# Kernel tuning notes

Hardware: AMD Instinct MI355X
Metric: run time of the kernel (lower is better)

## Reference

```python
import jax, jax.numpy as jnp
import numpy as np

N_HEAD = 16
N_KV_HEAD = 4
HEAD_DIM = 128
EPS = 1e-6


def apply_rotary_emb(x, cos, sin):
    # x: (B,T,H,hd); cos/sin: (1,T,1,hd//2)
    d = x.shape[3] // 2
    x1, x2 = x[..., :d], x[..., d:]
    y1 = x1 * cos + x2 * sin
    y2 = x1 * -sin + x2 * cos
    return jnp.concatenate([y1, y2], axis=3).astype(x.dtype)


def rmsnorm(x):
    # flax nnx.RMSNorm with use_scale=False: x * rsqrt(mean(x^2) + eps)
    ms = jnp.mean(jnp.square(x), axis=-1, keepdims=True)
    return (x * jax.lax.rsqrt(ms + EPS)).astype(x.dtype)


def setup_inputs() -> dict:
    key = jax.random.key(0)
    ks = jax.random.split(key, 7)
    B, T, C = 4, 2048, 2048
    s = 0.02
    return {
        "x": jax.random.normal(ks[0], (B, T, C), jnp.float32),
        "cos": jax.random.normal(ks[1], (1, T, 1, HEAD_DIM // 2), jnp.float32),
        "sin": jax.random.normal(ks[2], (1, T, 1, HEAD_DIM // 2), jnp.float32),
        "Wq": jax.random.normal(ks[3], (C, N_HEAD * HEAD_DIM), jnp.float32) * s,
        "Wk": jax.random.normal(ks[4], (C, N_KV_HEAD * HEAD_DIM), jnp.float32) * s,
        "Wv": jax.random.normal(ks[5], (C, N_KV_HEAD * HEAD_DIM), jnp.float32) * s,
        "Wo": jax.random.normal(ks[6], (C, C), jnp.float32) * s,
    }


def reference(x, cos, sin, Wq, Wk, Wv, Wo):
    B, T, C = x.shape
    q = (x @ Wq).reshape(B, T, N_HEAD, HEAD_DIM)
    k = (x @ Wk).reshape(B, T, N_KV_HEAD, HEAD_DIM)
    v = (x @ Wv).reshape(B, T, N_KV_HEAD, HEAD_DIM)
    q = rmsnorm(apply_rotary_emb(q, cos, sin))
    k = rmsnorm(apply_rotary_emb(k, cos, sin))
    # (B,H,T,hd)
    q = jnp.transpose(q, (0, 2, 1, 3))
    k = jnp.transpose(k, (0, 2, 1, 3))
    v = jnp.transpose(v, (0, 2, 1, 3))
    nrep = N_HEAD // N_KV_HEAD
    k = jnp.repeat(k, nrep, axis=1)
    v = jnp.repeat(v, nrep, axis=1)
    scale = 1.0 / jnp.sqrt(jnp.float32(HEAD_DIM))
    att = jnp.einsum('bhqd,bhkd->bhqk', q, k) * scale
    mask = jnp.tril(jnp.ones((T, T), dtype=bool))[None, None, :, :]
    att = jnp.where(mask, att, -jnp.inf)
    att = jax.nn.softmax(att, axis=-1)
    y = jnp.einsum('bhqk,bhkd->bhqd', att, v)
    y = jnp.transpose(y, (0, 2, 1, 3)).reshape(B, T, -1)
    return y @ Wo
```

## Files before the change

### kernel.cpp

```cpp
#include <hip/hip_runtime.h>
#include <hip/hip_bf16.h>

typedef __attribute__((ext_vector_type(8))) short short8;
typedef __attribute__((ext_vector_type(4))) float f32x4;
typedef __attribute__((ext_vector_type(16))) float f32x16;

#define B_SZ 4
#define T_SEQ 2048
#define C_DIM 2048
#define NH 16
#define NKV 4
#define HD 128

#define MFMA16 __builtin_amdgcn_mfma_f32_16x16x32_bf16
#define MFMA32 __builtin_amdgcn_mfma_f32_32x32x16_bf16

__device__ __forceinline__ unsigned short f2bf(float f) {
  union { __hip_bfloat16 h; unsigned short u; } v;
  v.h = __float2bfloat16(f);
  return v.u;
}
__device__ __forceinline__ float bf2f(unsigned short u) {
  union { unsigned short u; __hip_bfloat16 h; } v;
  v.u = u;
  return __bfloat162float(v.h);
}
__device__ __forceinline__ unsigned pkbf(float lo, float hi) {
  return (unsigned)f2bf(lo) | ((unsigned)f2bf(hi) << 16);
}

__device__ __forceinline__ void gload_lds16(const unsigned short* g, unsigned short* l) {
  __builtin_amdgcn_global_load_lds(
      (const __attribute__((address_space(1))) unsigned int*)g,
      (__attribute__((address_space(3))) unsigned int*)l, 16, 0, 0);
}

__global__ void prep(const float* __restrict__ x, unsigned short* __restrict__ xb,
                     const float* __restrict__ Wq, const float* __restrict__ Wk,
                     const float* __restrict__ Wv, const float* __restrict__ Wo,
                     unsigned short* __restrict__ WqkvT, unsigned short* __restrict__ WoT) {
  int bid = blockIdx.x, tid = threadIdx.x;
  if (bid < 16384) {
    int i = bid * 256 + tid;
    float4 f = ((const float4*)x)[i];
    ushort4 u = make_ushort4(f2bf(f.x), f2bf(f.y), f2bf(f.z), f2bf(f.w));
    ((ushort4*)xb)[i] = u;
    return;
  }
  __shared__ float tile[32][33];
  int idx = bid - 16384;
  int y = idx >> 6, kx = idx & 63;
  const float* W;
  unsigned short* Wt;
  int N, n0;
  if (y < 64) { W = Wq; Wt = WqkvT; N = 2048; n0 = y * 32; }
  else if (y < 80) { W = Wk; Wt = WqkvT + (size_t)2048 * 2048; N = 512; n0 = (y - 64) * 32; }
  else if (y < 96) { W = Wv; Wt = WqkvT + (size_t)2560 * 2048; N = 512; n0 = (y - 80) * 32; }
  else { W = Wo; Wt = WoT; N = 2048; n0 = (y - 96) * 32; }
  int k0 = kx * 32;
  int tx = tid & 31, ty = tid >> 5;
#pragma unroll
  for (int i = 0; i < 4; i++)
    tile[ty + i * 8][tx] = W[(size_t)(k0 + ty + i * 8) * N + n0 + tx];
  __syncthreads();
#pragma unroll
  for (int i = 0; i < 4; i++)
    Wt[(size_t)(n0 + ty + i * 8) * 2048 + k0 + tx] = f2bf(tile[tx][ty + i * 8]);
}

__global__ void vtrans(const unsigned short* __restrict__ qkv, unsigned short* __restrict__ Vt) {
  __shared__ unsigned short tile[32][34];
  int t0 = blockIdx.x * 32, d0 = blockIdx.y * 32;
  int b = blockIdx.z >> 2, kvh = blockIdx.z & 3;
  int tx = threadIdx.x, ty = threadIdx.y;
#pragma unroll
  for (int i = 0; i < 4; i++)
    tile[ty + i * 8][tx] =
        qkv[(size_t)(b * T_SEQ + t0 + ty + i * 8) * 3072 + 2560 + kvh * HD + d0 + tx];
  __syncthreads();
#pragma unroll
  for (int i = 0; i < 4; i++)
    Vt[((size_t)(b * NKV + kvh) * HD + d0 + ty + i * 8) * T_SEQ + t0 + tx] = tile[tx][ty + i * 8];
}

template <typename OutT>
__global__ __launch_bounds__(512, 2) void gemm128(const unsigned short* __restrict__ A,
                                                  const unsigned short* __restrict__ Bt,
                                                  OutT* __restrict__ Cc, int N, int K, int GX) {
  __shared__ alignas(16) unsigned short lds[2][3][128 * 64];
  const int tid = threadIdx.x, lane = tid & 63, wid = tid >> 6;
  const int wave_m = wid >> 2, wave_n = wid & 3;
  const int r16 = lane & 15, q4 = lane >> 4;
  const int sw = r16 & 7;

  int nwg = gridDim.x, orig = blockIdx.x;
  int qq = nwg >> 3, rr = nwg & 7;
  int xcd = orig & 7, loc = orig >> 3;
  int wg = (xcd < rr ? xcd * (qq + 1) : rr * (qq + 1) + (xcd - rr) * qq) + loc;
  int bx = wg % GX, by = wg / GX;
  const size_t row0 = (size_t)bx * 128, col0 = (size_t)by * 256;

  const unsigned short* Ab = A + row0 * K;
  const unsigned short* Bb0 = Bt + col0 * K;
  const unsigned short* Bb1 = Bt + (col0 + 128) * K;

  const int srow = lane >> 3, spb = lane & 7;
  auto stage = [&](const unsigned short* base, int buf, int slot, int k0) {
#pragma unroll
    for (int j = 0; j < 2; ++j) {
      int cw = j * 8 + wid;
      int row = cw * 8 + srow;
      gload_lds16(base + (size_t)row * K + k0 + ((spb ^ srow) * 8), &lds[buf][slot][cw * 512]);
    }
  };

  f32x4 acc[4][4];
  f32x4 zero = {0.f, 0.f, 0.f, 0.f};
#pragma unroll
  for (int m = 0; m < 4; m++)
#pragma unroll
    for (int n = 0; n < 4; n++) acc[m][n] = zero;

  const int NT = K / 64;
  stage(Ab, 0, 0, 0);
  stage(Bb0, 0, 1, 0);
  stage(Bb1, 0, 2, 0);
  stage(Ab, 1, 0, 64);
  asm volatile("s_waitcnt vmcnt(2)" ::: "memory");
  __builtin_amdgcn_s_barrier();

  short8 af[4][2], b01[2][2], b23[2][2];
  const int bslot = 1 + (wave_n >> 1);
  const int bro = (wave_n & 1) * 64;

  int cur = 0;
#pragma unroll 1
  for (int t = 0; t < NT; ++t) {
    const unsigned short* Ah = &lds[cur][0][0];
    const unsigned short* Bh = &lds[cur][bslot][0];
    const int k1 = t * 64 + 64, k2 = t * 64 + 128;
#pragma unroll
    for (int mf = 0; mf < 4; mf++)
#pragma unroll
      for (int kk = 0; kk < 2; kk++)
        af[mf][kk] =
            *(const short8*)(Ah + (wave_m * 64 + mf * 16 + r16) * 64 + (((kk * 4 + q4) ^ sw) * 8));
#pragma unroll
    for (int nf = 0; nf < 2; nf++)
#pragma unroll
      for (int kk = 0; kk < 2; kk++)
        b01[nf][kk] =
            *(const short8*)(Bh + (bro + nf * 16 + r16) * 64 + (((kk * 4 + q4) ^ sw) * 8));
    if (t + 1 < NT) stage(Bb0, cur ^ 1, 1, k1);
    __builtin_amdgcn_s_barrier();
    asm volatile("s_waitcnt lgkmcnt(0)" ::: "memory");
    __builtin_amdgcn_s_setprio(1);
#pragma unroll
    for (int mf = 0; mf < 4; mf++)
#pragma unroll
      for (int nf = 0; nf < 2; nf++)
#pragma unroll
        for (int kk = 0; kk < 2; kk++)
          acc[mf][nf] = MFMA16(af[mf][kk], b01[nf][kk], acc[mf][nf], 0, 0, 0);
    __builtin_amdgcn_s_setprio(0);
    __builtin_amdgcn_s_barrier();
#pragma unroll
    for (int nf = 0; nf < 2; nf++)
#pragma unroll
      for (int kk = 0; kk < 2; kk++)
        b23[nf][kk] =
            *(const short8*)(Bh + (bro + (nf + 2) * 16 + r16) * 64 + (((kk * 4 + q4) ^ sw) * 8));
    if (t + 1 < NT) stage(Bb1, cur ^ 1, 2, k1);
    if (t + 2 < NT) stage(Ab, cur, 0, k2);
    __builtin_amdgcn_s_barrier();
    asm volatile("s_waitcnt lgkmcnt(0)" ::: "memory");
    __builtin_amdgcn_s_setprio(1);
#pragma unroll
    for (int mf = 0; mf < 4; mf++)
#pragma unroll
      for (int nf = 0; nf < 2; nf++)
#pragma unroll
        for (int kk = 0; kk < 2; kk++)
          acc[mf][nf + 2] = MFMA16(af[mf][kk], b23[nf][kk], acc[mf][nf + 2], 0, 0, 0);
    __builtin_amdgcn_s_setprio(0);
    if (t + 2 < NT)
      asm volatile("s_waitcnt vmcnt(2)" ::: "memory");
    else if (t + 1 < NT)
      asm volatile("s_waitcnt vmcnt(0)" ::: "memory");
    __builtin_amdgcn_s_barrier();
    cur ^= 1;
  }

#pragma unroll
  for (int mf = 0; mf < 4; mf++)
#pragma unroll
    for (int nf = 0; nf < 4; nf++) {
      size_t rbase = row0 + wave_m * 64 + mf * 16 + q4 * 4;
      size_t cc = col0 + wave_n * 64 + nf * 16 + r16;
#pragma unroll
      for (int jj = 0; jj < 4; jj++) {
        if constexpr (sizeof(OutT) == 2)
          Cc[(rbase + jj) * (size_t)N + cc] = f2bf(acc[mf][nf][jj]);
        else
          Cc[(rbase + jj) * (size_t)N + cc] = acc[mf][nf][jj];
      }
    }
}

template <typename OutT>
__global__ __launch_bounds__(512, 2) void gemm256(const unsigned short* __restrict__ A,
                                                  const unsigned short* __restrict__ Bt,
                                                  OutT* __restrict__ Cc, int N, int K, int GX) {
  __shared__ alignas(16) unsigned short lds[2][4][128 * 64];
  const int tid = threadIdx.x, lane = tid & 63, wid = tid >> 6;
  const int wave_m = wid >> 2, wave_n = wid & 3;
  const int r16 = lane & 15, q4 = lane >> 4;
  const int sw = r16 & 7;

  int nwg = gridDim.x, orig = blockIdx.x;
  int qq = nwg >> 3, rr = nwg & 7;
  int xcd = orig & 7, loc = orig >> 3;
  int wg = (xcd < rr ? xcd * (qq + 1) : rr * (qq + 1) + (xcd - rr) * qq) + loc;
  int bx = wg % GX, by = wg / GX;
  const size_t row0 = (size_t)bx * 256, col0 = (size_t)by * 256;

  const unsigned short* Ab0 = A + row0 * K;
  const unsigned short* Ab1 = A + (row0 + 128) * K;
  const unsigned short* Bb0 = Bt + col0 * K;
  const unsigned short* Bb1 = Bt + (col0 + 128) * K;

  const int srow = lane >> 3, spb = lane & 7;
  auto stage = [&](const unsigned short* base, int buf, int slot, int k0) {
#pragma unroll
    for (int j = 0; j < 2; ++j) {
      int cw = j * 8 + wid;
      int row = cw * 8 + srow;
      gload_lds16(base + (size_t)row * K + k0 + ((spb ^ srow) * 8), &lds[buf][slot][cw * 512]);
    }
  };

  f32x4 acc[8][4];
  f32x4 zero = {0.f, 0.f, 0.f, 0.f};
#pragma unroll
  for (int m = 0; m < 8; m++)
#pragma unroll
    for (int n = 0; n < 4; n++) acc[m][n] = zero;

  const int NT = K / 64;
  stage(Ab0, 0, 0, 0);
  stage(Ab1, 0, 1, 0);
  stage(Bb0, 0, 2, 0);
  stage(Bb1, 0, 3, 0);
  stage(Ab0, 1, 0, 64);
  stage(Ab1, 1, 1, 64);
  asm volatile("s_waitcnt vmcnt(4)" ::: "memory");
  __builtin_amdgcn_s_barrier();

  short8 af[4][2], b01[2][2], b23[2][2];
  const int bslot = 2 + (wave_n >> 1);
  const int bro = (wave_n & 1) * 64;

  int cur = 0;
#pragma unroll 1
  for (int t = 0; t < NT; ++t) {
    const unsigned short* Ah = &lds[cur][wave_m][0];
    const unsigned short* Bh = &lds[cur][bslot][0];
    const int k1 = t * 64 + 64, k2 = t * 64 + 128;
#pragma unroll
    for (int mf = 0; mf < 4; mf++)
#pragma unroll
      for (int kk = 0; kk < 2; kk++)
        af[mf][kk] = *(const short8*)(Ah + (mf * 16 + r16) * 64 + (((kk * 4 + q4) ^ sw) * 8));
#pragma unroll
    for (int nf = 0; nf < 2; nf++)
#pragma unroll
      for (int kk = 0; kk < 2; kk++)
        b01[nf][kk] =
            *(const short8*)(Bh + (bro + nf * 16 + r16) * 64 + (((kk * 4 + q4) ^ sw) * 8));
    if (t + 1 < NT) stage(Bb0, cur ^ 1, 2, k1);
    __builtin_amdgcn_s_barrier();
    asm volatile("s_waitcnt lgkmcnt(0)" ::: "memory");
    __builtin_amdgcn_s_setprio(1);
#pragma unroll
    for (int mf = 0; mf < 4; mf++)
#pragma unroll
      for (int nf = 0; nf < 2; nf++)
#pragma unroll
        for (int kk = 0; kk < 2; kk++)
          acc[mf][nf] = MFMA16(af[mf][kk], b01[nf][kk], acc[mf][nf], 0, 0, 0);
    __builtin_amdgcn_s_setprio(0);
    __builtin_amdgcn_s_barrier();
#pragma unroll
    for (int nf = 0; nf < 2; nf++)
#pragma unroll
      for (int kk = 0; kk < 2; kk++)
        b23[nf][kk] =
            *(const short8*)(Bh + (bro + (nf + 2) * 16 + r16) * 64 + (((kk * 4 + q4) ^ sw) * 8));
    if (t + 1 < NT) stage(Bb1, cur ^ 1, 3, k1);
    __builtin_amdgcn_s_barrier();
    asm volatile("s_waitcnt lgkmcnt(0)" ::: "memory");
    __builtin_amdgcn_s_setprio(1);
#pragma unroll
    for (int mf = 0; mf < 4; mf++)
#pragma unroll
      for (int nf = 0; nf < 2; nf++)
#pragma unroll
        for (int kk = 0; kk < 2; kk++)
          acc[mf][nf + 2] = MFMA16(af[mf][kk], b23[nf][kk], acc[mf][nf + 2], 0, 0, 0);
    __builtin_amdgcn_s_setprio(0);
    __builtin_amdgcn_s_barrier();
#pragma unroll
    for (int mf = 0; mf < 4; mf++)
#pragma unroll
      for (int kk = 0; kk < 2; kk++)
        af[mf][kk] =
            *(const short8*)(Ah + ((mf + 4) * 16 + r16) * 64 + (((kk * 4 + q4) ^ sw) * 8));
    __builtin_amdgcn_s_barrier();
    asm volatile("s_waitcnt lgkmcnt(0)" ::: "memory");
    __builtin_amdgcn_s_setprio(1);
#pragma unroll
    for (int mf = 0; mf < 4; mf++)
#pragma unroll
      for (int nf = 0; nf < 2; nf++)
#pragma unroll
        for (int kk = 0; kk < 2; kk++)
          acc[mf + 4][nf] = MFMA16(af[mf][kk], b01[nf][kk], acc[mf + 4][nf], 0, 0, 0);
    __builtin_amdgcn_s_setprio(0);
    __builtin_amdgcn_s_barrier();
    if (t + 2 < NT) {
      stage(Ab0, cur, 0, k2);
      stage(Ab1, cur, 1, k2);
    }
    __builtin_amdgcn_s_barrier();
    __builtin_amdgcn_s_setprio(1);
#pragma unroll
    for (int mf = 0; mf < 4; mf++)
#pragma unroll
      for (int nf = 0; nf < 2; nf++)
#pragma unroll
        for (int kk = 0; kk < 2; kk++)
          acc[mf + 4][nf + 2] = MFMA16(af[mf][kk], b23[nf][kk], acc[mf + 4][nf + 2], 0, 0, 0);
    __builtin_amdgcn_s_setprio(0);
    if (t + 1 < NT) {
      if (t + 2 < NT)
        asm volatile("s_waitcnt vmcnt(4)" ::: "memory");
      else
        asm volatile("s_waitcnt vmcnt(0)" ::: "memory");
    }
    __builtin_amdgcn_s_barrier();
    cur ^= 1;
  }

#pragma unroll
  for (int mf = 0; mf < 8; mf++)
#pragma unroll
    for (int nf = 0; nf < 4; nf++) {
      size_t rbase = row0 + wave_m * 128 + mf * 16 + q4 * 4;
      size_t cc = col0 + wave_n * 64 + nf * 16 + r16;
#pragma unroll
      for (int jj = 0; jj < 4; jj++) {
        if constexpr (sizeof(OutT) == 2)
          Cc[(rbase + jj) * (size_t)N + cc] = f2bf(acc[mf][nf][jj]);
        else
          Cc[(rbase + jj) * (size_t)N + cc] = acc[mf][nf][jj];
      }
    }
}

__global__ void ropeAll(const unsigned short* __restrict__ qkv, const float* __restrict__ cosp,
                        const float* __restrict__ sinp, unsigned short* __restrict__ Qb,
                        unsigned short* __restrict__ Kb) {
  int gid = blockIdx.x * 4 + (threadIdx.x >> 6);
  int lane = threadIdx.x & 63;
  int hh = gid % 20;
  int bt = gid / 20;
  int t = bt % T_SEQ, b = bt / T_SEQ;
  int colbase;
  unsigned short* dst;
  float outscale;
  if (hh < 16) {
    colbase = hh * HD;
    dst = Qb + ((size_t)(b * NH + hh) * T_SEQ + t) * HD;
    outscale = 0.08838834764831845f;
  } else {
    int h2 = hh - 16;
    colbase = 2048 + h2 * HD;
    dst = Kb + ((size_t)(b * NKV + h2) * T_SEQ + t) * HD;
    outscale = 1.0f;
  }
  const unsigned short* src = qkv + (size_t)(b * T_SEQ + t) * 3072 + colbase;
  float x1 = bf2f(src[lane]), x2 = bf2f(src[64 + lane]);
  float c = cosp[t * 64 + lane], s = sinp[t * 64 + lane];
  float y1 = x1 * c + x2 * s;
  float y2 = x2 * c - x1 * s;
  float ss = y1 * y1 + y2 * y2;
#pragma unroll
  for (int d = 1; d < 64; d <<= 1) ss += __shfl_xor(ss, d);
  float r = rsqrtf(ss * (1.f / 128.f) + 1e-6f) * outscale;
  dst[lane] = f2bf(y1 * r);
  dst[64 + lane] = f2bf(y2 * r);
}

__global__ __launch_bounds__(256, 2) void attn(const unsigned short* __restrict__ Qn,
                                               const unsigned short* __restrict__ Kn,
                                               const unsigned short* __restrict__ Vt,
                                               unsigned short* __restrict__ Y) {
  __shared__ alignas(16) unsigned short lK[2][32 * 128];
  __shared__ alignas(16) unsigned short lV[2][128 * 32];

  int lin = blockIdx.x;
  int low3 = lin & 7, rest = lin >> 3;
  int chi = rest >> 6, idx = rest & 63;
  int c = (chi << 3) | low3;
  int b = c >> 2, kvh = c & 3;
  int h = kvh * 4 + (idx >> 4);
  int qt = 15 - (idx & 15);
  int Q0 = qt * 128;

  int lane = threadIdx.x & 63, w = threadIdx.x >> 6;
  const int q5 = lane & 31, hi = lane >> 5;
  const int qrow = Q0 + w * 32 + q5;
  const unsigned short* Qp = Qn + ((size_t)(b * NH + h) * T_SEQ + qrow) * HD;
  const unsigned short* Kp = Kn + (size_t)(b * NKV + kvh) * T_SEQ * HD;
  const unsigned short* Vp = Vt + (size_t)(b * NKV + kvh) * HD * T_SEQ;

  short8 qf[8];
#pragma unroll
  for (int i = 0; i < 8; i++) qf[i] = *(const short8*)(Qp + i * 16 + hi * 8);

  f32x16 o4[4];
#pragma unroll
  for (int d = 0; d < 4; d++)
#pragma unroll
    for (int r = 0; r < 16; r++) o4[d][r] = 0.f;
  float mrow = -1e30f, Lp = 0.f;

  auto stageK = [&](int kv0, int buf) {
#pragma unroll
    for (int j = 0; j < 2; ++j) {
      int cw = w * 2 + j;
      int gi = cw * 64 + lane;
      int slot = gi >> 5, krow = gi & 31;
      gload_lds16(Kp + (size_t)(kv0 + krow) * HD + slot * 8, &lK[buf][cw * 512]);
    }
  };
  auto stageV = [&](int kv0, int buf) {
#pragma unroll
    for (int j = 0; j < 2; ++j) {
      int cw = w * 2 + j;
      int gi = cw * 64 + lane;
      int cb = gi >> 7, vrow = gi & 127;
      gload_lds16(Vp + (size_t)vrow * T_SEQ + kv0 + cb * 8, &lV[buf][cw * 512]);
    }
  };

  const int ntiles = 4 * qt + 4;
  const int ntw = (Q0 + w * 32 + 63) >> 5;

  stageK(0, 0);
  stageV(0, 0);
  __syncthreads();
  int cur = 0;

  for (int t = 0; t < ntiles; ++t) {
    int kv0 = t * 32;
    if (t + 1 < ntiles) { stageK(kv0 + 32, cur ^ 1); stageV(kv0 + 32, cur ^ 1); }
    if (t < ntw) {
      f32x16 st;
#pragma unroll
      for (int r = 0; r < 16; r++) st[r] = 0.f;
      __builtin_amdgcn_s_setprio(1);
#pragma unroll
      for (int i = 0; i < 8; i++) {
        short8 kf = *(const short8*)(&lK[cur][((2 * i + hi) * 32 + q5) * 8]);
        st = MFMA32(kf, qf[i], st, 0, 0, 0);
      }
      __builtin_amdgcn_s_setprio(0);
      if (kv0 + 31 > Q0 + w * 32) {
#pragma unroll
        for (int r = 0; r < 16; r++) {
          int kg = kv0 + (r & 3) + 8 * (r >> 2) + 4 * hi;
          if (kg > qrow) st[r] = -1e30f;
        }
      }
      float pm = st[0];
#pragma unroll
      for (int r = 1; r < 16; r++) pm = fmaxf(pm, st[r]);
      pm = fmaxf(pm, __shfl_xor(pm, 32));
      if (!__all(pm - mrow <= 8.0f)) {
        float mn = fmaxf(mrow, pm);
        float al = __expf(mrow - mn);
        mrow = mn;
        Lp *= al;
#pragma unroll
        for (int d = 0; d < 4; d++)
#pragma unroll
          for (int r = 0; r < 16; r++) o4[d][r] *= al;
      }
      float p[16];
#pragma unroll
      for (int r = 0; r < 16; r++) {
        p[r] = __expf(st[r] - mrow);
        Lp += p[r];
      }
#pragma unroll
      for (int ks = 0; ks < 2; ks++) {
        unsigned x0 = pkbf(p[8 * ks + 0], p[8 * ks + 1]);
        unsigned x1 = pkbf(p[8 * ks + 2], p[8 * ks + 3]);
        unsigned y0 = pkbf(p[8 * ks + 4], p[8 * ks + 5]);
        unsigned y1 = pkbf(p[8 * ks + 6], p[8 * ks + 7]);
        unsigned sx0 = __shfl_xor((int)x0, 32), sx1 = __shfl_xor((int)x1, 32);
        unsigned sy0 = __shfl_xor((int)y0, 32), sy1 = __shfl_xor((int)y1, 32);
        union { unsigned u[4]; short8 s; } pw;
        pw.u[0] = hi ? sy0 : x0;
        pw.u[1] = hi ? sy1 : x1;
        pw.u[2] = hi ? y0 : sx0;
        pw.u[3] = hi ? y1 : sx1;
        const int cb = 2 * ks + hi;
        __builtin_amdgcn_s_setprio(1);
#pragma unroll
        for (int db = 0; db < 4; db++) {
          short8 vf = *(const short8*)(&lV[cur][(cb * 128 + db * 32 + q5) * 8]);
          o4[db] = MFMA32(vf, pw.s, o4[db], 0, 0, 0);
        }
        __builtin_amdgcn_s_setprio(0);
      }
    }
    __syncthreads();
    cur ^= 1;
  }

  float L = Lp + __shfl_xor(Lp, 32);
  float linv = 1.f / L;
  unsigned short* Yp = Y + ((size_t)(b * T_SEQ) + qrow) * (NH * HD) + h * HD;
#pragma unroll
  for (int db = 0; db < 4; db++)
#pragma unroll
    for (int g = 0; g < 4; g++) {
      int d0 = db * 32 + g * 8 + 4 * hi;
      ushort4 v = make_ushort4(f2bf(o4[db][g * 4 + 0] * linv), f2bf(o4[db][g * 4 + 1] * linv),
                               f2bf(o4[db][g * 4 + 2] * linv), f2bf(o4[db][g * 4 + 3] * linv));
      *(ushort4*)(Yp + d0) = v;
    }
}

extern "C" void kernel_launch(void* const* d_in, const int* in_sizes, int n_in,
                              void* d_out, int out_size, void* d_ws, size_t ws_size,
                              hipStream_t stream) {
  const float* x = (const float*)d_in[0];
  const float* cosp = (const float*)d_in[1];
  const float* sinp = (const float*)d_in[2];
  const float* Wq = (const float*)d_in[3];
  const float* Wk = (const float*)d_in[4];
  const float* Wv = (const float*)d_in[5];
  const float* Wo = (const float*)d_in[6];
  float* out = (float*)d_out;

  char* ws = (char*)d_ws;
  size_t off = 0;
  auto alloc = [&](size_t bytes) { void* p = ws + off; off += bytes; return p; };
  const size_t BT = (size_t)B_SZ * T_SEQ;
  unsigned short* xb = (unsigned short*)alloc(BT * C_DIM * 2);
  unsigned short* WqkvT = (unsigned short*)alloc((size_t)3072 * 2048 * 2);
  unsigned short* WoT = (unsigned short*)alloc((size_t)2048 * 2048 * 2);
  unsigned short* qkv = (unsigned short*)alloc(BT * 3072 * 2);
  unsigned short* Kb = (unsigned short*)alloc(BT * 512 * 2);
  unsigned short* Vb = (unsigned short*)alloc(BT * 512 * 2);
  unsigned short* Qb = xb;
  unsigned short* Yb = qkv;

  dim3 tb(32, 8);
  prep<<<26624, 256, 0, stream>>>(x, xb, Wq, Wk, Wv, Wo, WqkvT, WoT);

  gemm128<unsigned short><<<768, 512, 0, stream>>>(xb, WqkvT, qkv, 3072, 2048, 64);

  ropeAll<<<(B_SZ * T_SEQ * 20) / 4, 256, 0, stream>>>(qkv, cosp, sinp, Qb, Kb);
  vtrans<<<dim3(64, 4, 16), tb, 0, stream>>>(qkv, Vb);

  attn<<<dim3(1024), 256, 0, stream>>>(Qb, Kb, Vb, Yb);

  gemm256<float><<<256, 512, 0, stream>>>(Yb, WoT, out, 2048, 2048, 32);
}
```

Before: 404.5 us.

## Load attention K/V straight to registers and merge rope with V transpose

The attention kernel drops its LDS double-buffered K/V staging and block-wide barriers. Each wave now loads its own K and V fragments directly from global memory into registers and prefetches the next K tile during softmax. Each wave also loops only over its own causal tile count, not the block-wide count. Separately, the rope/norm kernel and the V transpose kernel are merged into one launch to save a launch. The trade-off is that the four waves sharing a KV head no longer share loads, so global/L2 traffic and register pressure rise.

```diff
diff --git a/kernel.cpp b/kernel.cpp
--- a/kernel.cpp
+++ b/kernel.cpp
@@ -68,21 +68,6 @@
     Wt[(size_t)(n0 + ty + i * 8) * 2048 + k0 + tx] = f2bf(tile[tx][ty + i * 8]);
 }
 
-__global__ void vtrans(const unsigned short* __restrict__ qkv, unsigned short* __restrict__ Vt) {
-  __shared__ unsigned short tile[32][34];
-  int t0 = blockIdx.x * 32, d0 = blockIdx.y * 32;
-  int b = blockIdx.z >> 2, kvh = blockIdx.z & 3;
-  int tx = threadIdx.x, ty = threadIdx.y;
-#pragma unroll
-  for (int i = 0; i < 4; i++)
-    tile[ty + i * 8][tx] =
-        qkv[(size_t)(b * T_SEQ + t0 + ty + i * 8) * 3072 + 2560 + kvh * HD + d0 + tx];
-  __syncthreads();
-#pragma unroll
-  for (int i = 0; i < 4; i++)
-    Vt[((size_t)(b * NKV + kvh) * HD + d0 + ty + i * 8) * T_SEQ + t0 + tx] = tile[tx][ty + i * 8];
-}
-
 template <typename OutT>
 __global__ __launch_bounds__(512, 2) void gemm128(const unsigned short* __restrict__ A,
                                                   const unsigned short* __restrict__ Bt,
@@ -367,47 +352,63 @@
     }
 }
 
-__global__ void ropeAll(const unsigned short* __restrict__ qkv, const float* __restrict__ cosp,
-                        const float* __restrict__ sinp, unsigned short* __restrict__ Qb,
-                        unsigned short* __restrict__ Kb) {
-  int gid = blockIdx.x * 4 + (threadIdx.x >> 6);
-  int lane = threadIdx.x & 63;
-  int hh = gid % 20;
-  int bt = gid / 20;
-  int t = bt % T_SEQ, b = bt / T_SEQ;
-  int colbase;
-  unsigned short* dst;
-  float outscale;
-  if (hh < 16) {
-    colbase = hh * HD;
-    dst = Qb + ((size_t)(b * NH + hh) * T_SEQ + t) * HD;
-    outscale = 0.08838834764831845f;
-  } else {
-    int h2 = hh - 16;
-    colbase = 2048 + h2 * HD;
-    dst = Kb + ((size_t)(b * NKV + h2) * T_SEQ + t) * HD;
-    outscale = 1.0f;
+__global__ void ropevt(const unsigned short* __restrict__ qkv, const float* __restrict__ cosp,
+                       const float* __restrict__ sinp, unsigned short* __restrict__ Qb,
+                       unsigned short* __restrict__ Kb, unsigned short* __restrict__ Vt) {
+  int bid = blockIdx.x, tid = threadIdx.x;
+  if (bid < 40960) {
+    int gid = bid * 4 + (tid >> 6);
+    int lane = tid & 63;
+    int hh = gid % 20;
+    int bt = gid / 20;
+    int t = bt % T_SEQ, b = bt / T_SEQ;
+    int colbase;
+    unsigned short* dst;
+    float outscale;
+    if (hh < 16) {
+      colbase = hh * HD;
+      dst = Qb + ((size_t)(b * NH + hh) * T_SEQ + t) * HD;
+      outscale = 0.08838834764831845f;
+    } else {
+      int h2 = hh - 16;
+      colbase = 2048 + h2 * HD;
+      dst = Kb + ((size_t)(b * NKV + h2) * T_SEQ + t) * HD;
+      outscale = 1.0f;
+    }
+    const unsigned short* src = qkv + (size_t)(b * T_SEQ + t) * 3072 + colbase;
+    float x1 = bf2f(src[lane]), x2 = bf2f(src[64 + lane]);
+    float c = cosp[t * 64 + lane], s = sinp[t * 64 + lane];
+    float y1 = x1 * c + x2 * s;
+    float y2 = x2 * c - x1 * s;
+    float ss = y1 * y1 + y2 * y2;
+#pragma unroll
+    for (int d = 1; d < 64; d <<= 1) ss += __shfl_xor(ss, d);
+    float r = rsqrtf(ss * (1.f / 128.f) + 1e-6f) * outscale;
+    dst[lane] = f2bf(y1 * r);
+    dst[64 + lane] = f2bf(y2 * r);
+    return;
   }
-  const unsigned short* src = qkv + (size_t)(b * T_SEQ + t) * 3072 + colbase;
-  float x1 = bf2f(src[lane]), x2 = bf2f(src[64 + lane]);
-  float c = cosp[t * 64 + lane], s = sinp[t * 64 + lane];
-  float y1 = x1 * c + x2 * s;
-  float y2 = x2 * c - x1 * s;
-  float ss = y1 * y1 + y2 * y2;
-#pragma unroll
-  for (int d = 1; d < 64; d <<= 1) ss += __shfl_xor(ss, d);
-  float r = rsqrtf(ss * (1.f / 128.f) + 1e-6f) * outscale;
-  dst[lane] = f2bf(y1 * r);
-  dst[64 + lane] = f2bf(y2 * r);
+  __shared__ unsigned short tile[32][34];
+  int idx = bid - 40960;
+  int xg = idx & 63, rem = idx >> 6;
+  int yg = rem & 3, zg = rem >> 2;
+  int t0 = xg * 32, d0 = yg * 32;
+  int b = zg >> 2, kvh = zg & 3;
+  int tx = tid & 31, ty = tid >> 5;
+#pragma unroll
+  for (int i = 0; i < 4; i++)
+    tile[ty + i * 8][tx] =
+        qkv[(size_t)(b * T_SEQ + t0 + ty + i * 8) * 3072 + 2560 + kvh * HD + d0 + tx];
+  __syncthreads();
+#pragma unroll
+  for (int i = 0; i < 4; i++)
+    Vt[((size_t)(b * NKV + kvh) * HD + d0 + ty + i * 8) * T_SEQ + t0 + tx] = tile[tx][ty + i * 8];
 }
 
 __global__ __launch_bounds__(256, 2) void attn(const unsigned short* __restrict__ Qn,
                                                const unsigned short* __restrict__ Kn,
                                                const unsigned short* __restrict__ Vt,
                                                unsigned short* __restrict__ Y) {
-  __shared__ alignas(16) unsigned short lK[2][32 * 128];
-  __shared__ alignas(16) unsigned short lV[2][128 * 32];
-
   int lin = blockIdx.x;
   int low3 = lin & 7, rest = lin >> 3;
   int chi = rest >> 6, idx = rest & 63;
@@ -435,99 +436,82 @@
     for (int r = 0; r < 16; r++) o4[d][r] = 0.f;
   float mrow = -1e30f, Lp = 0.f;
 
-  auto stageK = [&](int kv0, int buf) {
-#pragma unroll
-    for (int j = 0; j < 2; ++j) {
-      int cw = w * 2 + j;
-      int gi = cw * 64 + lane;
-      int slot = gi >> 5, krow = gi & 31;
-      gload_lds16(Kp + (size_t)(kv0 + krow) * HD + slot * 8, &lK[buf][cw * 512]);
-    }
+  short8 kreg[8];
+  auto loadK = [&](int kv0) {
+    const unsigned short* kp = Kp + (size_t)(kv0 + q5) * HD + hi * 8;
+#pragma unroll
+    for (int i = 0; i < 8; i++) kreg[i] = *(const short8*)(kp + i * 16);
   };
-  auto stageV = [&](int kv0, int buf) {
-#pragma unroll
-    for (int j = 0; j < 2; ++j) {
-      int cw = w * 2 + j;
-      int gi = cw * 64 + lane;
-      int cb = gi >> 7, vrow = gi & 127;
-      gload_lds16(Vp + (size_t)vrow * T_SEQ + kv0 + cb * 8, &lV[buf][cw * 512]);
+  short8 vreg[8];
+  auto loadV = [&](int kv0) {
+#pragma unroll
+    for (int db = 0; db < 4; db++) {
+      const unsigned short* vp = Vp + (size_t)(db * 32 + q5) * T_SEQ + kv0 + hi * 8;
+#pragma unroll
+      for (int ks = 0; ks < 2; ks++) vreg[db * 2 + ks] = *(const short8*)(vp + ks * 16);
     }
   };
 
-  const int ntiles = 4 * qt + 4;
   const int ntw = (Q0 + w * 32 + 63) >> 5;
 
-  stageK(0, 0);
-  stageV(0, 0);
-  __syncthreads();
-  int cur = 0;
-
-  for (int t = 0; t < ntiles; ++t) {
+  loadK(0);
+  for (int t = 0; t < ntw; ++t) {
     int kv0 = t * 32;
-    if (t + 1 < ntiles) { stageK(kv0 + 32, cur ^ 1); stageV(kv0 + 32, cur ^ 1); }
-    if (t < ntw) {
-      f32x16 st;
-#pragma unroll
-      for (int r = 0; r < 16; r++) st[r] = 0.f;
+    f32x16 st;
+#pragma unroll
+    for (int r = 0; r < 16; r++) st[r] = 0.f;
+    __builtin_amdgcn_s_setprio(1);
+#pragma unroll
+    for (int i = 0; i < 8; i++) st = MFMA32(kreg[i], qf[i], st, 0, 0, 0);
+    __builtin_amdgcn_s_setprio(0);
+    loadV(kv0);
+    if (kv0 + 31 > Q0 + w * 32) {
+#pragma unroll
+      for (int r = 0; r < 16; r++) {
+        int kg = kv0 + (r & 3) + 8 * (r >> 2) + 4 * hi;
+        if (kg > qrow) st[r] = -1e30f;
+      }
+    }
+    float pm = st[0];
+#pragma unroll
+    for (int r = 1; r < 16; r++) pm = fmaxf(pm, st[r]);
+    pm = fmaxf(pm, __shfl_xor(pm, 32));
+    if (!__all(pm - mrow <= 8.0f)) {
+      float mn = fmaxf(mrow, pm);
+      float al = __expf(mrow - mn);
+      mrow = mn;
+      Lp *= al;
+#pragma unroll
+      for (int d = 0; d < 4; d++)
+#pragma unroll
+        for (int r = 0; r < 16; r++) o4[d][r] *= al;
+    }
+    float p[16];
+#pragma unroll
+    for (int r = 0; r < 16; r++) {
+      p[r] = __expf(st[r] - mrow);
+      Lp += p[r];
+    }
+    if (t + 1 < ntw) loadK(kv0 + 32);
+#pragma unroll
+    for (int ks = 0; ks < 2; ks++) {
+      unsigned x0 = pkbf(p[8 * ks + 0], p[8 * ks + 1]);
+      unsigned x1 = pkbf(p[8 * ks + 2], p[8 * ks + 3]);
+      unsigned y0 = pkbf(p[8 * ks + 4], p[8 * ks + 5]);
+      unsigned y1 = pkbf(p[8 * ks + 6], p[8 * ks + 7]);
+      unsigned sx0 = __shfl_xor((int)x0, 32), sx1 = __shfl_xor((int)x1, 32);
+      unsigned sy0 = __shfl_xor((int)y0, 32), sy1 = __shfl_xor((int)y1, 32);
+      union { unsigned u[4]; short8 s; } pw;
+      pw.u[0] = hi ? sy0 : x0;
+      pw.u[1] = hi ? sy1 : x1;
+      pw.u[2] = hi ? y0 : sx0;
+      pw.u[3] = hi ? y1 : sx1;
       __builtin_amdgcn_s_setprio(1);
 #pragma unroll
-      for (int i = 0; i < 8; i++) {
-        short8 kf = *(const short8*)(&lK[cur][((2 * i + hi) * 32 + q5) * 8]);
-        st = MFMA32(kf, qf[i], st, 0, 0, 0);
-      }
+      for (int db = 0; db < 4; db++)
+        o4[db] = MFMA32(vreg[db * 2 + ks], pw.s, o4[db], 0, 0, 0);
       __builtin_amdgcn_s_setprio(0);
-      if (kv0 + 31 > Q0 + w * 32) {
-#pragma unroll
-        for (int r = 0; r < 16; r++) {
-          int kg = kv0 + (r & 3) + 8 * (r >> 2) + 4 * hi;
-          if (kg > qrow) st[r] = -1e30f;
-        }
-      }
-      float pm = st[0];
-#pragma unroll
-      for (int r = 1; r < 16; r++) pm = fmaxf(pm, st[r]);
-      pm = fmaxf(pm, __shfl_xor(pm, 32));
-      if (!__all(pm - mrow <= 8.0f)) {
-        float mn = fmaxf(mrow, pm);
-        float al = __expf(mrow - mn);
-        mrow = mn;
-        Lp *= al;
-#pragma unroll
-        for (int d = 0; d < 4; d++)
-#pragma unroll
-          for (int r = 0; r < 16; r++) o4[d][r] *= al;
-      }
-      float p[16];
-#pragma unroll
-      for (int r = 0; r < 16; r++) {
-        p[r] = __expf(st[r] - mrow);
-        Lp += p[r];
-      }
-#pragma unroll
-      for (int ks = 0; ks < 2; ks++) {
-        unsigned x0 = pkbf(p[8 * ks + 0], p[8 * ks + 1]);
-        unsigned x1 = pkbf(p[8 * ks + 2], p[8 * ks + 3]);
-        unsigned y0 = pkbf(p[8 * ks + 4], p[8 * ks + 5]);
-        unsigned y1 = pkbf(p[8 * ks + 6], p[8 * ks + 7]);
-        unsigned sx0 = __shfl_xor((int)x0, 32), sx1 = __shfl_xor((int)x1, 32);
-        unsigned sy0 = __shfl_xor((int)y0, 32), sy1 = __shfl_xor((int)y1, 32);
-        union { unsigned u[4]; short8 s; } pw;
-        pw.u[0] = hi ? sy0 : x0;
-        pw.u[1] = hi ? sy1 : x1;
-        pw.u[2] = hi ? y0 : sx0;
-        pw.u[3] = hi ? y1 : sx1;
-        const int cb = 2 * ks + hi;
-        __builtin_amdgcn_s_setprio(1);
-#pragma unroll
-        for (int db = 0; db < 4; db++) {
-          short8 vf = *(const short8*)(&lV[cur][(cb * 128 + db * 32 + q5) * 8]);
-          o4[db] = MFMA32(vf, pw.s, o4[db], 0, 0, 0);
-        }
-        __builtin_amdgcn_s_setprio(0);
-      }
-    }
-    __syncthreads();
-    cur ^= 1;
+    }
   }
 
   float L = Lp + __shfl_xor(Lp, 32);
@@ -569,13 +553,11 @@
   unsigned short* Qb = xb;
   unsigned short* Yb = qkv;
 
-  dim3 tb(32, 8);
   prep<<<26624, 256, 0, stream>>>(x, xb, Wq, Wk, Wv, Wo, WqkvT, WoT);
 
   gemm128<unsigned short><<<768, 512, 0, stream>>>(xb, WqkvT, qkv, 3072, 2048, 64);
 
-  ropeAll<<<(B_SZ * T_SEQ * 20) / 4, 256, 0, stream>>>(qkv, cosp, sinp, Qb, Kb);
-  vtrans<<<dim3(64, 4, 16), tb, 0, stream>>>(qkv, Vb);
+  ropevt<<<45056, 256, 0, stream>>>(qkv, cosp, sinp, Qb, Kb, Vb);
 
   attn<<<dim3(1024), 256, 0, stream>>>(Qb, Kb, Vb, Yb);
 
```

After: 579.5 us. 1.43x slower.
